# Optimization experiments

Hardware: AMD Instinct MI355X
Metric: run time of the kernel (lower is better)

## Reference

```python
import jax, jax.numpy as jnp
import numpy as np

DIM = 768
HEADS = 12
HEAD_DIM = DIM // HEADS
SCALE = HEAD_DIM ** -0.5


def setup_inputs() -> dict:
    key = jax.random.key(0)
    ks = jax.random.split(key, 8)
    B, N, C = 8, 1024, DIM
    s = 0.02
    return {
        "x": jax.random.normal(ks[0], (B, N, C), jnp.float32),
        "y": jax.random.normal(ks[1], (B, N, C), jnp.float32),
        "x_qkv_w": jax.random.normal(ks[2], (3 * C, C), jnp.float32) * s,
        "y_qkv_w": jax.random.normal(ks[3], (3 * C, C), jnp.float32) * s,
        "x_proj_w": jax.random.normal(ks[4], (C, C), jnp.float32) * s,
        "x_proj_b": jnp.zeros((C,), jnp.float32),
        "y_proj_w": jax.random.normal(ks[5], (C, C), jnp.float32) * s,
        "y_proj_b": jnp.zeros((C,), jnp.float32),
    }


def _split_qkv(t, qkv_w):
    # t: [B,N,C] -> q,k,v each [B,H,N,D]
    B, N, C = t.shape
    qkv = t @ qkv_w.T                      # [B,N,3C]
    qkv = qkv.reshape(B, N, 3, HEADS, HEAD_DIM).transpose(2, 0, 3, 1, 4)
    return qkv[0], qkv[1], qkv[2]


def reference(x, y, x_qkv_w, y_qkv_w, x_proj_w, x_proj_b, y_proj_w, y_proj_b):
    B, N, C = x.shape
    x_q, x_k, x_v = _split_qkv(x, x_qkv_w)
    y_q, y_k, y_v = _split_qkv(y, y_qkv_w)

    # scores: [B,H,N,N]; dropout is identity (attn_drop=0)
    x_attn = jax.nn.softmax(jnp.einsum('bhnd,bhmd->bhnm', x_q * SCALE, x_k), axis=-1)
    y_attn = jax.nn.softmax(jnp.einsum('bhnd,bhmd->bhnm', y_q * SCALE, y_k), axis=-1)

    # swapped V aggregation: x-branch attends over y_v, y-branch over x_v
    x_out = jnp.einsum('bhnm,bhmd->bhnd', x_attn, y_v).transpose(0, 2, 1, 3).reshape(B, N, C)
    y_out = jnp.einsum('bhnm,bhmd->bhnd', y_attn, x_v).transpose(0, 2, 1, 3).reshape(B, N, C)

    x_out = x_out @ x_proj_w.T + x_proj_b
    y_out = y_out @ y_proj_w.T + y_proj_b
    return (x_out, y_out)
```

## Files before the change

kernel.cpp:

```cpp
#include <hip/hip_runtime.h>
#include <hip/hip_bf16.h>
#include <stdint.h>
#include <stddef.h>

typedef unsigned short u16;
typedef __attribute__((ext_vector_type(8))) short bf16x8;
typedef __attribute__((ext_vector_type(4))) short bf16x4;
typedef __attribute__((ext_vector_type(4))) float f32x4;
typedef __attribute__((ext_vector_type(16))) float f32x16;
typedef __attribute__((ext_vector_type(4))) unsigned short u16x4;

#define MFMA_BF16 __builtin_amdgcn_mfma_f32_16x16x32_bf16
#define MFMA32    __builtin_amdgcn_mfma_f32_32x32x16_bf16

#if defined(__has_builtin)
#if __has_builtin(__builtin_amdgcn_exp2f)
#define EXP2F(x) __builtin_amdgcn_exp2f(x)
#endif
#endif
#ifndef EXP2F
#define EXP2F(x) __expf((x) * 0.6931471805599453f)
#endif

__device__ __forceinline__ void pl32swap(unsigned& a, unsigned& b) {
#if defined(__has_builtin) && __has_builtin(__builtin_amdgcn_permlane32_swap)
  typedef int v2i __attribute__((ext_vector_type(2)));
  v2i r = __builtin_amdgcn_permlane32_swap((int)a, (int)b, false, false);
  a = (unsigned)r.x;
  b = (unsigned)r.y;
#else
  asm volatile("v_permlane32_swap_b32 %0, %1" : "+v"(a), "+v"(b));
#endif
}

#define BAR_FULL asm volatile("s_waitcnt vmcnt(0)\n\ts_barrier" ::: "memory")

#define QSCALE 0.18033688011112042f

__device__ __forceinline__ u16 f2b(float x) {
  uint32_t u = __builtin_bit_cast(uint32_t, x);
  return (u16)((u + 0x7fffu + ((u >> 16) & 1u)) >> 16);
}

__device__ __forceinline__ unsigned pk2(float a, float b) {
  union { __hip_bfloat162 h; unsigned u; } c;
  c.h = __float22bfloat162_rn(make_float2(a, b));
  return c.u;
}

__device__ __forceinline__ void async16(const void* g, void* l) {
  __builtin_amdgcn_global_load_lds((const __attribute__((address_space(1))) void*)g,
                                   (__attribute__((address_space(3))) void*)l, 16, 0, 0);
}

__global__ void cvt_all(const float* __restrict__ x, const float* __restrict__ y,
                        const float* __restrict__ xqw, const float* __restrict__ yqw,
                        const float* __restrict__ xpw, const float* __restrict__ ypw,
                        u16* __restrict__ dst) {
  long i = ((long)blockIdx.x * 256 + threadIdx.x) * 4;
  const float* src;
  long off;
  if (i < 6291456)       { src = x;   off = 0; }
  else if (i < 12582912) { src = y;   off = 6291456; }
  else if (i < 14352384) { src = xqw; off = 12582912; }
  else if (i < 16121856) { src = yqw; off = 14352384; }
  else if (i < 16711680) { src = xpw; off = 16121856; }
  else                   { src = ypw; off = 16711680; }
  float4 v = *(const float4*)(src + (i - off));
  u16x4 o = { f2b(v.x), f2b(v.y), f2b(v.z), f2b(v.w) };
  *(u16x4*)(dst + i) = o;
}

__global__ __launch_bounds__(256, 2)
void qkv_gemm(const u16* __restrict__ Xb, const u16* __restrict__ Yb,
              const u16* __restrict__ Wx, const u16* __restrict__ Wy,
              u16* __restrict__ Qx, u16* __restrict__ Kx, u16* __restrict__ Vtx,
              u16* __restrict__ Qy, u16* __restrict__ Ky, u16* __restrict__ Vty) {
  __shared__ alignas(16) char smem[65536];
  const int br = blockIdx.z;
  const u16* A = br ? Yb : Xb;
  const u16* W = br ? Wy : Wx;
  u16* Qd = br ? Qy : Qx;
  u16* Kd = br ? Ky : Kx;
  u16* Vd = br ? Vty : Vtx;
  const int m0 = blockIdx.x * 128;
  const int j0 = blockIdx.y * 128;
  const int tid = threadIdx.x;
  const int wave = tid >> 6, lane = tid & 63;
  const int quad = lane >> 4, l16 = lane & 15;
  const int wm = wave >> 1, wn = wave & 1;
  const int srow = wave * 32 + (lane >> 3);
  const int scol = (((lane & 7) ^ ((lane >> 3) & 7)) * 8);
  const int l7 = l16 & 7;

  auto stage = [&](int k0, int p) {
#pragma unroll
    for (int c = 0; c < 4; ++c) {
      async16(A + (size_t)(m0 + srow + c * 8) * 768 + k0 + scol,
              smem + p * 16384 + wave * 4096 + c * 1024);
      async16(W + (size_t)(j0 + srow + c * 8) * 768 + k0 + scol,
              smem + 32768 + p * 16384 + wave * 4096 + c * 1024);
    }
  };

  f32x4 acc[4][4] = {};
  stage(0, 0);

  for (int kt = 0; kt < 12; ++kt) {
    const int p = kt & 1;
    BAR_FULL;
    if (kt < 11) stage((kt + 1) * 64, p ^ 1);
    const u16* Ap = (const u16*)smem + p * 8192;
    const u16* Bp = (const u16*)smem + 16384 + p * 8192;
#pragma unroll
    for (int kc = 0; kc < 2; ++kc) {
      bf16x8 af[4], bfr[4];
#pragma unroll
      for (int t = 0; t < 4; ++t) {
        af[t]  = *(const bf16x8*)&Ap[(wm * 64 + t * 16 + l16) * 64 + (((kc * 4 + quad) ^ l7) * 8)];
        bfr[t] = *(const bf16x8*)&Bp[(wn * 64 + t * 16 + l16) * 64 + (((kc * 4 + quad) ^ l7) * 8)];
      }
#pragma unroll
      for (int mt = 0; mt < 4; ++mt)
#pragma unroll
        for (int nt = 0; nt < 4; ++nt)
          acc[mt][nt] = MFMA_BF16(af[mt], bfr[nt], acc[mt][nt], 0, 0, 0);
    }
  }

  __syncthreads();
  u16* Ts = (u16*)smem;
  const int s3 = j0 / 768;

  if (s3 == 2) {
#pragma unroll
    for (int mt = 0; mt < 4; ++mt)
#pragma unroll
      for (int nt = 0; nt < 4; ++nt) {
        const int j = wn * 64 + nt * 16 + l16;
        const int mb = wm * 64 + mt * 16 + quad * 4;
        u16x4 pk = { f2b(acc[mt][nt][0]), f2b(acc[mt][nt][1]),
                     f2b(acc[mt][nt][2]), f2b(acc[mt][nt][3]) };
        *(u16x4*)&Ts[j * 136 + mb] = pk;
      }
    __syncthreads();
#pragma unroll
    for (int rt = 0; rt < 8; ++rt) {
      const int j = wave * 32 + rt * 4 + (lane >> 4);
      const int mo = (lane & 15) * 8;
      bf16x8 v = *(const bf16x8*)&Ts[j * 136 + mo];
      const int jr = j0 + j - 1536;
      const int h = jr >> 6, d = jr & 63;
      const int gm = m0 + mo;
      const int b = gm >> 10, n = gm & 1023;
      *(bf16x8*)&Vd[((size_t)(b * 12 + h) * 64 + d) * 1024 + n] = v;
    }
  } else {
    const float qs = s3 ? 1.0f : QSCALE;
#pragma unroll
    for (int mt = 0; mt < 4; ++mt)
#pragma unroll
      for (int nt = 0; nt < 4; ++nt) {
        const int j = wn * 64 + nt * 16 + l16;
#pragma unroll
        for (int r = 0; r < 4; ++r) {
          const int m = wm * 64 + mt * 16 + quad * 4 + r;
          Ts[m * 136 + j] = f2b(acc[mt][nt][r] * qs);
        }
      }
    __syncthreads();
    u16* Dd = s3 ? Kd : Qd;
#pragma unroll
    for (int rt = 0; rt < 8; ++rt) {
      const int m = wave * 32 + rt * 4 + (lane >> 4);
      const int jh = (lane >> 3) & 1, jo = (lane & 7) * 8;
      bf16x8 v = *(const bf16x8*)&Ts[m * 136 + jh * 64 + jo];
      const int jr = j0 + jh * 64 + jo - s3 * 768;
      const int h = jr >> 6, d = jr & 63;
      const int gm = m0 + m;
      const int b = gm >> 10, n = gm & 1023;
      *(bf16x8*)&Dd[((size_t)(b * 12 + h) * 1024 + n) * 64 + d] = v;
    }
  }
}

__global__ __launch_bounds__(256, 2)
void attn_kernel(const u16* __restrict__ Qx, const u16* __restrict__ Kx, const u16* __restrict__ Vtx,
                 const u16* __restrict__ Qy, const u16* __restrict__ Ky, const u16* __restrict__ Vty,
                 u16* __restrict__ Ox, u16* __restrict__ Oy) {
  __shared__ alignas(16) u16 Ks[2][64 * 64];
  __shared__ alignas(16) u16 Vs[2][64 * 64];
  const int br = blockIdx.z;
  const u16* Q = br ? Qy : Qx;
  const u16* K = br ? Ky : Kx;
  const u16* V = br ? Vtx : Vty;
  u16* O = br ? Oy : Ox;
  const int bh = blockIdx.y;
  const int q0 = blockIdx.x * 256;
  const int tid = threadIdx.x;
  const int wave = tid >> 6, lane = tid & 63;
  const int l = lane & 31, hi = lane >> 5;
  const int l7 = lane & 7;
  const int r8 = (lane >> 3) & 7;
  const int sw = ((lane & 7) ^ r8) * 8;

  const u16* Qb = Q + (size_t)bh * 65536;
  const u16* Kb = K + (size_t)bh * 65536;
  const u16* Vb = V + (size_t)bh * 65536;

  const int krow = wave * 16 + r8;

#pragma unroll
  for (int c = 0; c < 2; ++c) {
    async16(Kb + (size_t)(krow + c * 8) * 64 + sw, (char*)Ks[0] + wave * 2048 + c * 1024);
    async16(Vb + (size_t)(krow + c * 8) * 1024 + sw, (char*)Vs[0] + wave * 2048 + c * 1024);
  }

  bf16x8 qf[2][4];
#pragma unroll
  for (int qh = 0; qh < 2; ++qh)
#pragma unroll
    for (int dc = 0; dc < 4; ++dc)
      qf[qh][dc] = *(const bf16x8*)(Qb + (size_t)(q0 + wave * 64 + qh * 32 + l) * 64 + dc * 16 + hi * 8);

  f32x16 oacc[2][2] = {};
  float lsum[2] = {0.f, 0.f};

  union FrU { unsigned u[4]; bf16x8 v; };

  for (int it = 0; it < 16; ++it) {
    const int p = it & 1;
    BAR_FULL;
    if (it < 15) {
      const int kv1 = (it + 1) * 64;
#pragma unroll
      for (int c = 0; c < 2; ++c) {
        async16(Kb + (size_t)(kv1 + krow + c * 8) * 64 + sw, (char*)Ks[p ^ 1] + wave * 2048 + c * 1024);
        async16(Vb + (size_t)(krow + c * 8) * 1024 + kv1 + sw, (char*)Vs[p ^ 1] + wave * 2048 + c * 1024);
      }
    }

    const u16* Kp = Ks[p];
    const u16* Vp = Vs[p];

#pragma unroll
    for (int s = 0; s < 2; ++s) {
      bf16x8 kf[4];
#pragma unroll
      for (int dc = 0; dc < 4; ++dc)
        kf[dc] = *(const bf16x8*)&Kp[(s * 32 + l) * 64 + (((dc * 2 + hi) ^ l7) * 8)];

      FrU fragA[2][2];
#pragma unroll
      for (int qh = 0; qh < 2; ++qh) {
        f32x16 st = {};
#pragma unroll
        for (int dc = 0; dc < 4; ++dc)
          st = MFMA32(kf[dc], qf[qh][dc], st, 0, 0, 0);
        float pv[16];
#pragma unroll
        for (int r = 0; r < 16; ++r) pv[r] = EXP2F(st[r]);
        lsum[qh] += (((pv[0] + pv[1]) + (pv[2] + pv[3])) + ((pv[4] + pv[5]) + (pv[6] + pv[7])))
                  + (((pv[8] + pv[9]) + (pv[10] + pv[11])) + ((pv[12] + pv[13]) + (pv[14] + pv[15])));
        unsigned P[8];
#pragma unroll
        for (int i = 0; i < 8; ++i) P[i] = pk2(pv[2 * i], pv[2 * i + 1]);
#pragma unroll
        for (int f = 0; f < 2; ++f) {
          unsigned a0 = P[f * 4 + 0], b0 = P[f * 4 + 2];
          unsigned a1 = P[f * 4 + 1], b1 = P[f * 4 + 3];
          pl32swap(a0, b0);
          pl32swap(a1, b1);
          fragA[qh][f].u[0] = a0;
          fragA[qh][f].u[1] = a1;
          fragA[qh][f].u[2] = b0;
          fragA[qh][f].u[3] = b1;
        }
      }
#pragma unroll
      for (int f = 0; f < 2; ++f)
#pragma unroll
        for (int dt = 0; dt < 2; ++dt) {
          bf16x8 vf = *(const bf16x8*)&Vp[(dt * 32 + l) * 64 + (((s * 4 + f * 2 + hi) ^ l7) * 8)];
          oacc[0][dt] = MFMA32(fragA[0][f].v, vf, oacc[0][dt], 0, 0, 0);
          oacc[1][dt] = MFMA32(fragA[1][f].v, vf, oacc[1][dt], 0, 0, 0);
        }
    }
  }

  float* LS = (float*)Ks[0] + wave * 64;
  {
    float t0 = lsum[0] + __shfl_xor(lsum[0], 32, 64);
    float t1 = lsum[1] + __shfl_xor(lsum[1], 32, 64);
    LS[l] = 1.0f / t0;
    LS[32 + l] = 1.0f / t1;
  }
  __syncthreads();

  const int b = bh / 12, h = bh % 12;
#pragma unroll
  for (int qh = 0; qh < 2; ++qh)
#pragma unroll
    for (int r = 0; r < 16; ++r) {
      const int cr = (r & 3) + 8 * (r >> 2) + 4 * hi;
      const float iv = LS[qh * 32 + cr];
      const int qrow = q0 + wave * 64 + qh * 32 + cr;
      const size_t ob = ((size_t)(b * 1024 + qrow)) * 768 + h * 64;
#pragma unroll
      for (int dt = 0; dt < 2; ++dt)
        O[ob + dt * 32 + l] = f2b(oacc[qh][dt][r] * iv);
    }
}

__global__ __launch_bounds__(256, 2)
void proj_gemm(const u16* __restrict__ Ox, const u16* __restrict__ Oy,
               const u16* __restrict__ Pxw, const u16* __restrict__ Pyw,
               const float* __restrict__ bx, const float* __restrict__ by,
               float* __restrict__ out) {
  __shared__ alignas(16) char smem[65536];
  const int br = blockIdx.z;
  const u16* A = br ? Oy : Ox;
  const u16* W = br ? Pyw : Pxw;
  const float* bias = br ? by : bx;
  float* op = out + (size_t)br * 6291456;
  const int m0 = blockIdx.x * 128;
  const int j0 = blockIdx.y * 128;
  const int tid = threadIdx.x;
  const int wave = tid >> 6, lane = tid & 63;
  const int quad = lane >> 4, l16 = lane & 15;
  const int wm = wave >> 1, wn = wave & 1;
  const int srow = wave * 32 + (lane >> 3);
  const int scol = (((lane & 7) ^ ((lane >> 3) & 7)) * 8);
  const int l7 = l16 & 7;

  auto stage = [&](int k0, int p) {
#pragma unroll
    for (int c = 0; c < 4; ++c) {
      async16(A + (size_t)(m0 + srow + c * 8) * 768 + k0 + scol,
              smem + p * 16384 + wave * 4096 + c * 1024);
      async16(W + (size_t)(j0 + srow + c * 8) * 768 + k0 + scol,
              smem + 32768 + p * 16384 + wave * 4096 + c * 1024);
    }
  };

  f32x4 acc[4][4] = {};
  stage(0, 0);

  for (int kt = 0; kt < 12; ++kt) {
    const int p = kt & 1;
    BAR_FULL;
    if (kt < 11) stage((kt + 1) * 64, p ^ 1);
    const u16* Ap = (const u16*)smem + p * 8192;
    const u16* Bp = (const u16*)smem + 16384 + p * 8192;
#pragma unroll
    for (int kc = 0; kc < 2; ++kc) {
      bf16x8 af[4], bfr[4];
#pragma unroll
      for (int t = 0; t < 4; ++t) {
        af[t]  = *(const bf16x8*)&Ap[(wm * 64 + t * 16 + l16) * 64 + (((kc * 4 + quad) ^ l7) * 8)];
        bfr[t] = *(const bf16x8*)&Bp[(wn * 64 + t * 16 + l16) * 64 + (((kc * 4 + quad) ^ l7) * 8)];
      }
#pragma unroll
      for (int mt = 0; mt < 4; ++mt)
#pragma unroll
        for (int nt = 0; nt < 4; ++nt)
          acc[mt][nt] = MFMA_BF16(af[mt], bfr[nt], acc[mt][nt], 0, 0, 0);
    }
  }

#pragma unroll
  for (int mt = 0; mt < 4; ++mt) {
#pragma unroll
    for (int nt = 0; nt < 4; ++nt) {
      const int j = j0 + wn * 64 + nt * 16 + l16;
      const float bj = bias[j];
#pragma unroll
      for (int r = 0; r < 4; ++r) {
        const int m = m0 + wm * 64 + mt * 16 + quad * 4 + r;
        op[(size_t)m * 768 + j] = acc[mt][nt][r] + bj;
      }
    }
  }
}

extern "C" void kernel_launch(void* const* d_in, const int* in_sizes, int n_in,
                              void* d_out, int out_size, void* d_ws, size_t ws_size,
                              hipStream_t stream) {
  (void)in_sizes; (void)n_in; (void)out_size; (void)ws_size;
  const float* x   = (const float*)d_in[0];
  const float* y   = (const float*)d_in[1];
  const float* xqw = (const float*)d_in[2];
  const float* yqw = (const float*)d_in[3];
  const float* xpw = (const float*)d_in[4];
  const float* xpb = (const float*)d_in[5];
  const float* ypw = (const float*)d_in[6];
  const float* ypb = (const float*)d_in[7];
  float* out = (float*)d_out;

  char* p = (char*)d_ws;
  u16* Xb  = (u16*)p; p += 12582912;
  u16* Yb  = (u16*)p; p += 12582912;
  u16* Wxb = (u16*)p; p += 3538944;
  u16* Wyb = (u16*)p; p += 3538944;
  u16* Pxb = (u16*)p; p += 1179648;
  u16* Pyb = (u16*)p; p += 1179648;
  u16* Qx  = (u16*)p; p += 12582912;
  u16* Kx  = (u16*)p; p += 12582912;
  u16* Vtx = (u16*)p; p += 12582912;
  u16* Qy  = (u16*)p; p += 12582912;
  u16* Ky  = (u16*)p; p += 12582912;
  u16* Vty = (u16*)p; p += 12582912;
  u16* Ox  = Xb;
  u16* Oy  = Yb;

  cvt_all<<<16896, 256, 0, stream>>>(x, y, xqw, yqw, xpw, ypw, Xb);

  qkv_gemm<<<dim3(64, 18, 2), 256, 0, stream>>>(Xb, Yb, Wxb, Wyb,
                                                Qx, Kx, Vtx, Qy, Ky, Vty);
  attn_kernel<<<dim3(4, 96, 2), 256, 0, stream>>>(Qx, Kx, Vtx, Qy, Ky, Vty, Ox, Oy);
  proj_gemm<<<dim3(64, 6, 2), 256, 0, stream>>>(Ox, Oy, Pxb, Pyb, xpb, ypb, out);
}
```

Before: 277.1 us.

## Halve attention query tile per block and reorder grid with heads fastest

Each attention block now covers 128 query rows (32 per wave) instead of 256, doubling the grid to 1536 blocks. The grid is reordered so batch-head is the fastest-varying dimension, and the barrier before the normalisation step is dropped because each wave reads only its own LDS slot. The aim is to shrink the tail when blocks run in uneven waves across CUs and to cut per-wave register pressure. The cost is twice as much K/V traffic per query row and only one reuse of each V fragment per MFMA pair.

```diff
diff --git a/kernel.cpp b/kernel.cpp
--- a/kernel.cpp
+++ b/kernel.cpp
@@ -195,8 +195,8 @@
   const u16* K = br ? Ky : Kx;
   const u16* V = br ? Vtx : Vty;
   u16* O = br ? Oy : Ox;
-  const int bh = blockIdx.y;
-  const int q0 = blockIdx.x * 256;
+  const int bh = blockIdx.x;
+  const int q0 = blockIdx.y * 128;
   const int tid = threadIdx.x;
   const int wave = tid >> 6, lane = tid & 63;
   const int l = lane & 31, hi = lane >> 5;
@@ -216,15 +216,13 @@
     async16(Vb + (size_t)(krow + c * 8) * 1024 + sw, (char*)Vs[0] + wave * 2048 + c * 1024);
   }
 
-  bf16x8 qf[2][4];
-#pragma unroll
-  for (int qh = 0; qh < 2; ++qh)
-#pragma unroll
-    for (int dc = 0; dc < 4; ++dc)
-      qf[qh][dc] = *(const bf16x8*)(Qb + (size_t)(q0 + wave * 64 + qh * 32 + l) * 64 + dc * 16 + hi * 8);
-
-  f32x16 oacc[2][2] = {};
-  float lsum[2] = {0.f, 0.f};
+  bf16x8 qf[4];
+#pragma unroll
+  for (int dc = 0; dc < 4; ++dc)
+    qf[dc] = *(const bf16x8*)(Qb + (size_t)(q0 + wave * 32 + l) * 64 + dc * 16 + hi * 8);
+
+  f32x16 oacc[2] = {};
+  float lsum = 0.f;
 
   union FrU { unsigned u[4]; bf16x8 v; };
 
@@ -250,66 +248,57 @@
       for (int dc = 0; dc < 4; ++dc)
         kf[dc] = *(const bf16x8*)&Kp[(s * 32 + l) * 64 + (((dc * 2 + hi) ^ l7) * 8)];
 
-      FrU fragA[2][2];
-#pragma unroll
-      for (int qh = 0; qh < 2; ++qh) {
-        f32x16 st = {};
-#pragma unroll
-        for (int dc = 0; dc < 4; ++dc)
-          st = MFMA32(kf[dc], qf[qh][dc], st, 0, 0, 0);
-        float pv[16];
-#pragma unroll
-        for (int r = 0; r < 16; ++r) pv[r] = EXP2F(st[r]);
-        lsum[qh] += (((pv[0] + pv[1]) + (pv[2] + pv[3])) + ((pv[4] + pv[5]) + (pv[6] + pv[7])))
-                  + (((pv[8] + pv[9]) + (pv[10] + pv[11])) + ((pv[12] + pv[13]) + (pv[14] + pv[15])));
-        unsigned P[8];
-#pragma unroll
-        for (int i = 0; i < 8; ++i) P[i] = pk2(pv[2 * i], pv[2 * i + 1]);
-#pragma unroll
-        for (int f = 0; f < 2; ++f) {
-          unsigned a0 = P[f * 4 + 0], b0 = P[f * 4 + 2];
-          unsigned a1 = P[f * 4 + 1], b1 = P[f * 4 + 3];
-          pl32swap(a0, b0);
-          pl32swap(a1, b1);
-          fragA[qh][f].u[0] = a0;
-          fragA[qh][f].u[1] = a1;
-          fragA[qh][f].u[2] = b0;
-          fragA[qh][f].u[3] = b1;
-        }
+      f32x16 st = {};
+#pragma unroll
+      for (int dc = 0; dc < 4; ++dc)
+        st = MFMA32(kf[dc], qf[dc], st, 0, 0, 0);
+      float pv[16];
+#pragma unroll
+      for (int r = 0; r < 16; ++r) pv[r] = EXP2F(st[r]);
+      lsum += (((pv[0] + pv[1]) + (pv[2] + pv[3])) + ((pv[4] + pv[5]) + (pv[6] + pv[7])))
+            + (((pv[8] + pv[9]) + (pv[10] + pv[11])) + ((pv[12] + pv[13]) + (pv[14] + pv[15])));
+      unsigned P[8];
+#pragma unroll
+      for (int i = 0; i < 8; ++i) P[i] = pk2(pv[2 * i], pv[2 * i + 1]);
+      FrU fragA[2];
+#pragma unroll
+      for (int f = 0; f < 2; ++f) {
+        unsigned a0 = P[f * 4 + 0], b0 = P[f * 4 + 2];
+        unsigned a1 = P[f * 4 + 1], b1 = P[f * 4 + 3];
+        pl32swap(a0, b0);
+        pl32swap(a1, b1);
+        fragA[f].u[0] = a0;
+        fragA[f].u[1] = a1;
+        fragA[f].u[2] = b0;
+        fragA[f].u[3] = b1;
       }
 #pragma unroll
       for (int f = 0; f < 2; ++f)
 #pragma unroll
         for (int dt = 0; dt < 2; ++dt) {
           bf16x8 vf = *(const bf16x8*)&Vp[(dt * 32 + l) * 64 + (((s * 4 + f * 2 + hi) ^ l7) * 8)];
-          oacc[0][dt] = MFMA32(fragA[0][f].v, vf, oacc[0][dt], 0, 0, 0);
-          oacc[1][dt] = MFMA32(fragA[1][f].v, vf, oacc[1][dt], 0, 0, 0);
+          oacc[dt] = MFMA32(fragA[f].v, vf, oacc[dt], 0, 0, 0);
         }
     }
   }
 
-  float* LS = (float*)Ks[0] + wave * 64;
+  float* LS = (float*)Ks[0] + wave * 32;
   {
-    float t0 = lsum[0] + __shfl_xor(lsum[0], 32, 64);
-    float t1 = lsum[1] + __shfl_xor(lsum[1], 32, 64);
+    float t0 = lsum + __shfl_xor(lsum, 32, 64);
     LS[l] = 1.0f / t0;
-    LS[32 + l] = 1.0f / t1;
-  }
-  __syncthreads();
+  }
 
   const int b = bh / 12, h = bh % 12;
 #pragma unroll
-  for (int qh = 0; qh < 2; ++qh)
-#pragma unroll
-    for (int r = 0; r < 16; ++r) {
-      const int cr = (r & 3) + 8 * (r >> 2) + 4 * hi;
-      const float iv = LS[qh * 32 + cr];
-      const int qrow = q0 + wave * 64 + qh * 32 + cr;
-      const size_t ob = ((size_t)(b * 1024 + qrow)) * 768 + h * 64;
-#pragma unroll
-      for (int dt = 0; dt < 2; ++dt)
-        O[ob + dt * 32 + l] = f2b(oacc[qh][dt][r] * iv);
-    }
+  for (int r = 0; r < 16; ++r) {
+    const int cr = (r & 3) + 8 * (r >> 2) + 4 * hi;
+    const float iv = LS[cr];
+    const int qrow = q0 + wave * 32 + cr;
+    const size_t ob = ((size_t)(b * 1024 + qrow)) * 768 + h * 64;
+#pragma unroll
+    for (int dt = 0; dt < 2; ++dt)
+      O[ob + dt * 32 + l] = f2b(oacc[dt][r] * iv);
+  }
 }
 
 __global__ __launch_bounds__(256, 2)
@@ -417,6 +406,6 @@
 
   qkv_gemm<<<dim3(64, 18, 2), 256, 0, stream>>>(Xb, Yb, Wxb, Wyb,
                                                 Qx, Kx, Vtx, Qy, Ky, Vty);
-  attn_kernel<<<dim3(4, 96, 2), 256, 0, stream>>>(Qx, Kx, Vtx, Qy, Ky, Vty, Ox, Oy);
+  attn_kernel<<<dim3(96, 8, 2), 256, 0, stream>>>(Qx, Kx, Vtx, Qy, Ky, Vty, Ox, Oy);
   proj_gemm<<<dim3(64, 6, 2), 256, 0, stream>>>(Ox, Oy, Pxb, Pyb, xpb, ypb, out);
 }
```

After: 287.3 us. 3.7% more time.
